# Kernel tuning notes

Measured on AMD Instinct MI355X. Metric: run time of the kernel, lower is better.

## Reference

```python
import jax, jax.numpy as jnp
import numpy as np

N_E = 1024
E_DIM = 64


def setup_inputs() -> dict:
    key = jax.random.key(0)
    k_z, k_emb = jax.random.split(key)
    z = jax.random.normal(k_z, (8, 16, 32, 32, E_DIM), dtype=jnp.float32)
    embeddings = jax.random.normal(k_emb, (N_E, E_DIM), dtype=jnp.float32) * 0.02
    return {"z": z, "embeddings": embeddings}


def reference(z, embeddings):
    # flatten all leading dims: [B*T*H*W, e_dim]
    zf = z.reshape(-1, z.shape[-1])
    # squared L2 distance: ||z||^2 + ||e||^2 - 2 z.e  -> [tokens, n_e]
    d = (jnp.sum(zf ** 2, axis=1, keepdims=True)
         + jnp.sum(embeddings ** 2, axis=1)[None, :]
         - 2.0 * jnp.einsum('bd,nd->bn', zf, embeddings))
    idx = jnp.argmin(d, axis=1)
    z_q = embeddings[idx].reshape(z.shape)
    idx = idx.reshape(z.shape[:-1])
    return z_q, idx
```

## Files before the change

### kernel.cpp

```cpp
#include <hip/hip_runtime.h>

typedef short short8 __attribute__((ext_vector_type(8)));
typedef float f32x4 __attribute__((ext_vector_type(4)));

#define NTOK (8 * 16 * 32 * 32)
#define NE 1024
#define ED 64
#define TPB 256
#define MBLK 128
#define NMF 2
#define WKEY (1 << 18)
#define SCALE (-131072.0f)

__device__ __forceinline__ unsigned short bf16_rtne(float f) {
    unsigned u = __float_as_uint(f);
    return (unsigned short)((u + 0x7FFFu + ((u >> 16) & 1u)) >> 16);
}
__device__ __forceinline__ float bf16_to_f32(unsigned short h) {
    return __uint_as_float(((unsigned)h) << 16);
}

__device__ float exact_dist(const float* __restrict__ z, const float* __restrict__ emb,
                            int t, int e) {
    const float* zt = z + (size_t)t * ED;
    const float* ep = emb + (size_t)e * ED;
    float r0 = 0.f, r1 = 0.f, r2 = 0.f, r3 = 0.f;
    float r4 = 0.f, r5 = 0.f, r6 = 0.f, r7 = 0.f;
    for (int d = 0; d < ED; d += 8) {
        r0 += zt[d + 0] * zt[d + 0];
        r1 += zt[d + 1] * zt[d + 1];
        r2 += zt[d + 2] * zt[d + 2];
        r3 += zt[d + 3] * zt[d + 3];
        r4 += zt[d + 4] * zt[d + 4];
        r5 += zt[d + 5] * zt[d + 5];
        r6 += zt[d + 6] * zt[d + 6];
        r7 += zt[d + 7] * zt[d + 7];
    }
    float s1 = ((r0 + r1) + (r2 + r3)) + ((r4 + r5) + (r6 + r7));
    float q0 = 0.f, q1 = 0.f, q2 = 0.f, q3 = 0.f;
    float q4 = 0.f, q5 = 0.f, q6 = 0.f, q7 = 0.f;
    for (int d = 0; d < ED; d += 8) {
        float v0 = ep[d + 0], v1 = ep[d + 1], v2 = ep[d + 2], v3 = ep[d + 3];
        float v4 = ep[d + 4], v5 = ep[d + 5], v6 = ep[d + 6], v7 = ep[d + 7];
        q0 += v0 * v0; q1 += v1 * v1; q2 += v2 * v2; q3 += v3 * v3;
        q4 += v4 * v4; q5 += v5 * v5; q6 += v6 * v6; q7 += v7 * v7;
    }
    float s2 = ((q0 + q1) + (q2 + q3)) + ((q4 + q5) + (q6 + q7));
    float a0 = 0.f, a1 = 0.f, a2 = 0.f, a3 = 0.f;
    for (int d = 0; d < ED; d += 4) {
        a0 = fmaf(zt[d + 0], ep[d + 0], a0);
        a1 = fmaf(zt[d + 1], ep[d + 1], a1);
        a2 = fmaf(zt[d + 2], ep[d + 2], a2);
        a3 = fmaf(zt[d + 3], ep[d + 3], a3);
    }
    float g = (a0 + a1) + (a2 + a3);
    return (s1 + s2) - 2.0f * g;
}

__global__ __launch_bounds__(128) void vq_prep(
    const float* __restrict__ emb,
    unsigned short* __restrict__ bfH,
    unsigned short* __restrict__ bfL,
    float* __restrict__ s2s)
{
    const int f = blockIdx.x * 128 + threadIdx.x;
    const int col = f & 15;
    const int quad = (f >> 4) & 3;
    const int kb = (f >> 6) & 1;
    const int nt = f >> 7;
    const int e = nt * 16 + col;
    const int k0 = kb * 32 + quad * 8;

    const float* p = emb + (size_t)e * ED + k0;
    float4 v0 = *(const float4*)p;
    float4 v1 = *(const float4*)(p + 4);
    float vs[8] = {v0.x, v0.y, v0.z, v0.w, v1.x, v1.y, v1.z, v1.w};
    short8 h, l;
#pragma unroll
    for (int j = 0; j < 8; ++j) {
        float x = vs[j] * SCALE;
        unsigned short hb = bf16_rtne(x);
        float hf = bf16_to_f32(hb);
        unsigned short lb = bf16_rtne(x - hf);
        h[j] = (short)hb;
        l[j] = (short)lb;
    }
    *(short8*)&bfH[(size_t)f * 8] = h;
    *(short8*)&bfL[(size_t)f * 8] = l;

    if ((f & 7) == 0) {
        const int e2 = f >> 3;
        const float* ep = emb + (size_t)e2 * ED;
        float q0 = 0.f, q1 = 0.f, q2 = 0.f, q3 = 0.f;
        float q4 = 0.f, q5 = 0.f, q6 = 0.f, q7 = 0.f;
#pragma unroll
        for (int d = 0; d < ED; d += 8) {
            float w0 = ep[d + 0], w1 = ep[d + 1], w2 = ep[d + 2], w3 = ep[d + 3];
            float w4 = ep[d + 4], w5 = ep[d + 5], w6 = ep[d + 6], w7 = ep[d + 7];
            q0 += w0 * w0; q1 += w1 * w1; q2 += w2 * w2; q3 += w3 * w3;
            q4 += w4 * w4; q5 += w5 * w5; q6 += w6 * w6; q7 += w7 * w7;
        }
        float s2 = ((q0 + q1) + (q2 + q3)) + ((q4 + q5) + (q6 + q7));
        s2s[e2] = s2 * 65536.0f;
    }
}

__global__ void __launch_bounds__(TPB)
__attribute__((amdgpu_waves_per_eu(4, 4))) vq_main(
    const float* __restrict__ z,
    const float* __restrict__ emb,
    const unsigned short* __restrict__ bfH,
    const unsigned short* __restrict__ bfL,
    const float* __restrict__ s2s_g,
    float* __restrict__ zq_out,
    float* __restrict__ idx_out)
{
    __shared__ float s2L[NE];
    __shared__ int idx_lds[MBLK];

    const int tid = threadIdx.x;
    const int lane = tid & 63;
    const int wv = __builtin_amdgcn_readfirstlane(tid >> 6);
    const int col = lane & 15;
    const int quad = lane >> 4;
    const int blockTok = blockIdx.x * MBLK;

    for (int i = tid; i < NE; i += TPB) s2L[i] = s2s_g[i];

    short8 Ah[NMF][2], Al[NMF][2];
#pragma unroll
    for (int mf = 0; mf < NMF; ++mf) {
#pragma unroll
        for (int kf = 0; kf < 2; ++kf) {
            const float* zp = z + (size_t)(blockTok + wv * 32 + mf * 16 + col) * ED
                              + kf * 32 + quad * 8;
            float4 v0 = *(const float4*)zp;
            float4 v1 = *(const float4*)(zp + 4);
            float vs[8] = {v0.x, v0.y, v0.z, v0.w, v1.x, v1.y, v1.z, v1.w};
            short8 h, l;
#pragma unroll
            for (int j = 0; j < 8; ++j) {
                float x = vs[j];
                unsigned short hb = bf16_rtne(x);
                float hf = bf16_to_f32(hb);
                unsigned short lb = bf16_rtne(x - hf);
                h[j] = (short)hb;
                l[j] = (short)lb;
            }
            Ah[mf][kf] = h;
            Al[mf][kf] = l;
        }
    }

    int aK[NMF][4], bK[NMF][4];
#pragma unroll
    for (int mf = 0; mf < NMF; ++mf)
#pragma unroll
        for (int r = 0; r < 4; ++r) { aK[mf][r] = 0x7FFFFFFF; bK[mf][r] = 0x7FFFFFFF; }

    __syncthreads();

    const short8* bh8 = (const short8*)bfH;
    const short8* bl8 = (const short8*)bfL;

#pragma unroll 2
    for (int nt = 0; nt < 64; ++nt) {
        const int base = nt * 128 + lane;
        short8 Bh0 = bh8[base], Bh1 = bh8[base + 64];
        short8 Bl0 = bl8[base], Bl1 = bl8[base + 64];

        const float s2v = s2L[nt * 16 + col];
        const int e = nt * 16 + col;
#pragma unroll
        for (int mf = 0; mf < NMF; ++mf) {
            f32x4 cc = {s2v, s2v, s2v, s2v};
            cc = __builtin_amdgcn_mfma_f32_16x16x32_bf16(Ah[mf][0], Bh0, cc, 0, 0, 0);
            cc = __builtin_amdgcn_mfma_f32_16x16x32_bf16(Ah[mf][1], Bh1, cc, 0, 0, 0);
            cc = __builtin_amdgcn_mfma_f32_16x16x32_bf16(Al[mf][0], Bh0, cc, 0, 0, 0);
            cc = __builtin_amdgcn_mfma_f32_16x16x32_bf16(Al[mf][1], Bh1, cc, 0, 0, 0);
            cc = __builtin_amdgcn_mfma_f32_16x16x32_bf16(Ah[mf][0], Bl0, cc, 0, 0, 0);
            cc = __builtin_amdgcn_mfma_f32_16x16x32_bf16(Ah[mf][1], Bl1, cc, 0, 0, 0);
#pragma unroll
            for (int r = 0; r < 4; ++r) {
                int key = ((int)cc[r]) * 1024 + e;
                int t1 = min(aK[mf][r], key);
                bK[mf][r] = min(bK[mf][r], max(aK[mf][r], key));
                aK[mf][r] = t1;
            }
        }
    }

#pragma unroll
    for (int mf = 0; mf < NMF; ++mf) {
#pragma unroll
        for (int r = 0; r < 4; ++r) {
            const int a0 = aK[mf][r], b0 = bK[mf][r];
            int A = a0, B = b0;
#pragma unroll
            for (int off = 1; off < 16; off <<= 1) {
                int A2 = __shfl_xor(A, off);
                int B2 = __shfl_xor(B, off);
                int lo = min(A, A2), hi = max(A, A2);
                B = min(min(B, B2), hi);
                A = lo;
            }
            int winner = A & 1023;
            if (B - A <= WKEY) {
                const int t = blockTok + wv * 32 + mf * 16 + quad * 4 + r;
                float dbest = 3.4e38f;
                int ibest = 1 << 30;
                if (a0 <= A + WKEY) {
                    int e = a0 & 1023;
                    float d = exact_dist(z, emb, t, e);
                    if (d < dbest || (d == dbest && e < ibest)) { dbest = d; ibest = e; }
                }
                if (b0 <= A + WKEY) {
                    int e = b0 & 1023;
                    float d = exact_dist(z, emb, t, e);
                    if (d < dbest || (d == dbest && e < ibest)) { dbest = d; ibest = e; }
                }
#pragma unroll
                for (int off = 1; off < 16; off <<= 1) {
                    float d2 = __shfl_xor(dbest, off);
                    int i2 = __shfl_xor(ibest, off);
                    if (d2 < dbest || (d2 == dbest && i2 < ibest)) { dbest = d2; ibest = i2; }
                }
                winner = ibest;
            }
            if (col == 0) idx_lds[wv * 32 + mf * 16 + quad * 4 + r] = winner;
        }
    }

    __syncthreads();

    if (tid < MBLK) idx_out[blockTok + tid] = (float)idx_lds[tid];
    const float4* emb_f4 = (const float4*)emb;
    float4* zq_f4 = (float4*)zq_out;
#pragma unroll
    for (int i = 0; i < MBLK * 16 / TPB; ++i) {
        int item = tid + i * TPB;
        int tl = item >> 4, f4 = item & 15;
        int wi = idx_lds[tl];
        zq_f4[(size_t)(blockTok + tl) * 16 + f4] = emb_f4[(size_t)wi * 16 + f4];
    }
}

extern "C" void kernel_launch(void* const* d_in, const int* in_sizes, int n_in,
                              void* d_out, int out_size, void* d_ws, size_t ws_size,
                              hipStream_t stream) {
    const float* z = (const float*)d_in[0];
    const float* emb = (const float*)d_in[1];
    float* out = (float*)d_out;
    float* zq = out;
    float* idx = out + (size_t)NTOK * ED;

    char* ws = (char*)d_ws;
    float* s2s = (float*)ws;
    unsigned short* bfH = (unsigned short*)(ws + 4096);
    unsigned short* bfL = (unsigned short*)(ws + 4096 + 131072);

    vq_prep<<<64, 128, 0, stream>>>(emb, bfH, bfL, s2s);
    vq_main<<<NTOK / MBLK, TPB, 0, stream>>>(z, emb, bfH, bfL, s2s, zq, idx);
}
```

Before: 157.2 us.

## Stage codebook tiles through double-buffered LDS and vectorize norm precompute

The main kernel now loads each 16-entry codebook tile (high and low bf16 parts) cooperatively into a double-buffered shared-memory buffer, prefetching the next tile into registers while computing on the current one. Previously every wave read the tile directly from global memory. The aim is to cut redundant global/L2 traffic across the four waves and overlap loads with MFMA work. The cost is a block-wide barrier on every tile iteration and the loss of the earlier unroll. The prep kernel's embedding-norm computation is also rewritten to use four threads per row with float4 loads and shuffle reductions.

Result: faster. 151.2 us (-3.8%).

```diff
diff --git a/kernel.cpp b/kernel.cpp
--- a/kernel.cpp
+++ b/kernel.cpp
@@ -88,20 +88,17 @@
     *(short8*)&bfH[(size_t)f * 8] = h;
     *(short8*)&bfL[(size_t)f * 8] = l;
 
-    if ((f & 7) == 0) {
-        const int e2 = f >> 3;
-        const float* ep = emb + (size_t)e2 * ED;
-        float q0 = 0.f, q1 = 0.f, q2 = 0.f, q3 = 0.f;
-        float q4 = 0.f, q5 = 0.f, q6 = 0.f, q7 = 0.f;
-#pragma unroll
-        for (int d = 0; d < ED; d += 8) {
-            float w0 = ep[d + 0], w1 = ep[d + 1], w2 = ep[d + 2], w3 = ep[d + 3];
-            float w4 = ep[d + 4], w5 = ep[d + 5], w6 = ep[d + 6], w7 = ep[d + 7];
-            q0 += w0 * w0; q1 += w1 * w1; q2 += w2 * w2; q3 += w3 * w3;
-            q4 += w4 * w4; q5 += w5 * w5; q6 += w6 * w6; q7 += w7 * w7;
-        }
-        float s2 = ((q0 + q1) + (q2 + q3)) + ((q4 + q5) + (q6 + q7));
-        s2s[e2] = s2 * 65536.0f;
+    if (f < 4096) {
+        const int row = f >> 2;
+        const float4* rp = (const float4*)(emb + (size_t)row * ED + (f & 3) * 16);
+        float4 a = rp[0], b = rp[1], c = rp[2], d = rp[3];
+        float s = a.x * a.x + a.y * a.y + a.z * a.z + a.w * a.w
+                + b.x * b.x + b.y * b.y + b.z * b.z + b.w * b.w
+                + c.x * c.x + c.y * c.y + c.z * c.z + c.w * c.w
+                + d.x * d.x + d.y * d.y + d.z * d.z + d.w * d.w;
+        s += __shfl_xor(s, 1);
+        s += __shfl_xor(s, 2);
+        if ((f & 3) == 0) s2s[row] = s * 65536.0f;
     }
 }
 
@@ -117,6 +114,7 @@
 {
     __shared__ float s2L[NE];
     __shared__ int idx_lds[MBLK];
+    __shared__ uint4 Bbuf[2][256];
 
     const int tid = threadIdx.x;
     const int lane = tid & 63;
@@ -126,6 +124,10 @@
     const int blockTok = blockIdx.x * MBLK;
 
     for (int i = tid; i < NE; i += TPB) s2L[i] = s2s_g[i];
+
+    const uint4* src = (const uint4*)(tid < 128 ? bfH : bfL);
+    const int chunk = tid & 127;
+    const int dstc = (tid >> 7) * 128 + chunk;
 
     short8 Ah[NMF][2], Al[NMF][2];
 #pragma unroll
@@ -158,16 +160,19 @@
 #pragma unroll
         for (int r = 0; r < 4; ++r) { aK[mf][r] = 0x7FFFFFFF; bK[mf][r] = 0x7FFFFFFF; }
 
+    Bbuf[0][dstc] = src[chunk];
     __syncthreads();
 
-    const short8* bh8 = (const short8*)bfH;
-    const short8* bl8 = (const short8*)bfL;
-
-#pragma unroll 2
+    int p = 0;
     for (int nt = 0; nt < 64; ++nt) {
-        const int base = nt * 128 + lane;
-        short8 Bh0 = bh8[base], Bh1 = bh8[base + 64];
-        short8 Bl0 = bl8[base], Bl1 = bl8[base + 64];
+        uint4 nv;
+        if (nt < 63) nv = src[(nt + 1) * 128 + chunk];
+
+        const short8* bp = (const short8*)Bbuf[p];
+        short8 Bh0 = bp[lane];
+        short8 Bh1 = bp[64 + lane];
+        short8 Bl0 = bp[128 + lane];
+        short8 Bl1 = bp[192 + lane];
 
         const float s2v = s2L[nt * 16 + col];
         const int e = nt * 16 + col;
@@ -188,6 +193,10 @@
                 aK[mf][r] = t1;
             }
         }
+
+        if (nt < 63) Bbuf[p ^ 1][dstc] = nv;
+        __syncthreads();
+        p ^= 1;
     }
 
 #pragma unroll
```
